# Kernel tuning notes

Hardware: AMD Instinct MI355X
Metric: run time of the kernel (lower is better)

The kernel has to match this reference:

```python
import jax, jax.numpy as jnp
import numpy as np

SEQ, B, IN, H = 512, 64, 1024, 1024


def setup_inputs() -> dict:
    key = jax.random.key(0)
    ks = jax.random.split(key, 7)
    s = 1.0 / np.sqrt(H)
    return {
        "inp": jax.random.normal(ks[0], (SEQ, B, IN), dtype=jnp.float32),
        "h0": jax.random.normal(ks[1], (1, B, H), dtype=jnp.float32),
        "c0": jax.random.normal(ks[2], (1, B, H), dtype=jnp.float32),
        "W_ih": jax.random.uniform(ks[3], (4 * H, IN), jnp.float32, -s, s),
        "W_hh": jax.random.uniform(ks[4], (4 * H, H), jnp.float32, -s, s),
        "b_ih": jax.random.uniform(ks[5], (4 * H,), jnp.float32, -s, s),
        "b_hh": jax.random.uniform(ks[6], (4 * H,), jnp.float32, -s, s),
    }


def _lstm_scan(x_bsi, h, c, W_ih, W_hh, b_ih, b_hh):
    # Precompute input projections for all timesteps in one big GEMM: (B,S,4H)
    x_proj = jnp.einsum("bsi,gi->bsg", x_bsi, W_ih) + (b_ih + b_hh)

    def step(carry, xp):
        h, c = carry  # (B,H) each; xp: (B,4H)
        gates = xp + h @ W_hh.T
        i, f, g, o = jnp.split(gates, 4, axis=-1)
        c = jax.nn.sigmoid(f) * c + jax.nn.sigmoid(i) * jnp.tanh(g)
        h = jax.nn.sigmoid(o) * jnp.tanh(c)
        return (h, c), h

    (h, c), ys = jax.lax.scan(step, (h, c), jnp.swapaxes(x_proj, 0, 1))
    return ys, h, c  # ys: (S,B,H) with ys[t] = h_t


def reference(inp, h0, c0, W_ih, W_hh, b_ih, b_hh):
    seq_len, batch, _ = inp.shape
    # Faithful to torch: .view reshapes (memory reinterpretation), NOT transpose
    x = inp.reshape(batch, seq_len, -1)          # (B,S,I)
    h = h0.reshape(batch, -1)                    # (B,H)
    c = c0.reshape(batch, -1)                    # (B,H)
    ys, h, c = _lstm_scan(x, h, c, W_ih, W_hh, b_ih, b_hh)
    # torch builds output (B,S,H) with output[:, t] = h_t, then views to (S,B,H)
    output = jnp.swapaxes(ys, 0, 1).reshape(seq_len, batch, -1)
    return output, (h.reshape(-1, batch, H), c.reshape(-1, batch, H))
```

## Files before the change

### kernel.cpp

```cpp
#include <hip/hip_runtime.h>
#include <cstdint>


typedef __bf16 bf16x8 __attribute__((ext_vector_type(8)));
typedef __bf16 bf16x4 __attribute__((ext_vector_type(4)));
typedef float  floatx4 __attribute__((ext_vector_type(4)));

#define SEQ   512
#define BATCH 64
#define HID   1024
#define GATES 4096
#define TC    128

__device__ __forceinline__ float fast_sigm(float x) {
  return 1.0f / (1.0f + __expf(-x));
}
__device__ __forceinline__ float fast_tanh(float x) {
  x = fminf(15.0f, fmaxf(-15.0f, x));
  float e = __expf(2.0f * x);
  return (e - 1.0f) / (e + 1.0f);
}

__global__ void cast_f32_to_bf16_x4(const float* __restrict__ src,
                                    __bf16* __restrict__ dst, int n4) {
  int i = blockIdx.x * blockDim.x + threadIdx.x;
  if (i < n4) {
    float4 v = reinterpret_cast<const float4*>(src)[i];
    bf16x4 o;
    o[0] = (__bf16)v.x; o[1] = (__bf16)v.y; o[2] = (__bf16)v.z; o[3] = (__bf16)v.w;
    reinterpret_cast<bf16x4*>(dst)[i] = o;
  }
}

__global__ void bias_sum(const float* __restrict__ a, const float* __restrict__ b,
                         float* __restrict__ o) {
  int i = blockIdx.x * blockDim.x + threadIdx.x;
  if (i < GATES) o[i] = a[i] + b[i];
}

__global__ __launch_bounds__(256) void gemm_xproj(
    const __bf16* __restrict__ X,
    const __bf16* __restrict__ W,
    const float*  __restrict__ bias,
    float*        __restrict__ XP,
    int t0) {
  __shared__ __bf16 As[128][40];
  __shared__ __bf16 Bs[128][40];

  const int tid  = threadIdx.x;
  const int lane = tid & 63;
  const int w    = tid >> 6;
  const int wm   = w >> 1, wn = w & 1;
  const int mt   = blockIdx.x;
  const int n0   = blockIdx.y * 128;
  const long arow0 = (long)mt * 512 + t0;

  floatx4 acc[4][4] = {};

  for (int k0 = 0; k0 < 1024; k0 += 32) {
    __syncthreads();
#pragma unroll
    for (int r = 0; r < 2; ++r) {
      int c = tid + 256 * r;
      int row = c >> 2, c8 = c & 3;
      *reinterpret_cast<uint4*>(&As[row][c8 * 8]) =
          *reinterpret_cast<const uint4*>(&X[(arow0 + row) * 1024 + k0 + c8 * 8]);
      *reinterpret_cast<uint4*>(&Bs[row][c8 * 8]) =
          *reinterpret_cast<const uint4*>(&W[(long)(n0 + row) * 1024 + k0 + c8 * 8]);
    }
    __syncthreads();

    bf16x8 a[4], b[4];
#pragma unroll
    for (int i = 0; i < 4; ++i)
      a[i] = *reinterpret_cast<const __shared__ bf16x8*>(
          &As[wm * 64 + i * 16 + (lane & 15)][(lane >> 4) * 8]);
#pragma unroll
    for (int j = 0; j < 4; ++j)
      b[j] = *reinterpret_cast<const __shared__ bf16x8*>(
          &Bs[wn * 64 + j * 16 + (lane & 15)][(lane >> 4) * 8]);
#pragma unroll
    for (int i = 0; i < 4; ++i)
#pragma unroll
      for (int j = 0; j < 4; ++j)
        acc[i][j] = __builtin_amdgcn_mfma_f32_16x16x32_bf16(a[i], b[j], acc[i][j], 0, 0, 0);
  }

#pragma unroll
  for (int i = 0; i < 4; ++i) {
    int mloc = wm * 64 + i * 16 + (lane >> 4) * 4;
#pragma unroll
    for (int j = 0; j < 4; ++j) {
      int n = n0 + wn * 64 + j * 16 + (lane & 15);
      float bn = bias[n];
#pragma unroll
      for (int r = 0; r < 4; ++r)
        XP[(long)(mt * 128 + mloc + r) * 4096 + n] = acc[i][j][r] + bn;
    }
  }
}

__global__ __launch_bounds__(256) void lstm_step(
    const __bf16* __restrict__ hin,
    __bf16*       __restrict__ hout,
    float*        __restrict__ cst,
    const __bf16* __restrict__ Whh,
    const float*  __restrict__ xp,
    float*        __restrict__ out,
    int t) {
  __shared__ __bf16 Hs[16][1032];
  __shared__ __bf16 Bs[64][264];
  __shared__ float  Gs[4][16][17];

  const int tid  = threadIdx.x;
  const int lane = tid & 63;
  const int w    = tid >> 6;
  const int j0   = blockIdx.x * 16;
  const int b0   = blockIdx.y * 16;

#pragma unroll
  for (int r = 0; r < 8; ++r) {
    int c = tid + 256 * r;
    int row = c >> 7, c8 = c & 127;
    *reinterpret_cast<uint4*>(&Hs[row][c8 * 8]) =
        *reinterpret_cast<const uint4*>(&hin[(b0 + row) * 1024 + c8 * 8]);
  }

  floatx4 acc = {};
  for (int kc = 0; kc < 4; ++kc) {
    __syncthreads();
#pragma unroll
    for (int r = 0; r < 8; ++r) {
      int c = tid + 256 * r;
      int rb = c >> 5, c8 = c & 31;
      int grow = (rb >> 4) * 1024 + j0 + (rb & 15);
      *reinterpret_cast<uint4*>(&Bs[rb][c8 * 8]) =
          *reinterpret_cast<const uint4*>(&Whh[(long)grow * 1024 + kc * 256 + c8 * 8]);
    }
    __syncthreads();
#pragma unroll
    for (int q = 0; q < 8; ++q) {
      bf16x8 a = *reinterpret_cast<const __shared__ bf16x8*>(
          &Hs[lane & 15][kc * 256 + q * 32 + (lane >> 4) * 8]);
      bf16x8 b = *reinterpret_cast<const __shared__ bf16x8*>(
          &Bs[w * 16 + (lane & 15)][q * 32 + (lane >> 4) * 8]);
      acc = __builtin_amdgcn_mfma_f32_16x16x32_bf16(a, b, acc, 0, 0, 0);
    }
  }

#pragma unroll
  for (int r = 0; r < 4; ++r)
    Gs[w][(lane >> 4) * 4 + r][lane & 15] = acc[r];
  __syncthreads();

  int bb = tid >> 4, jj = tid & 15;
  int b = b0 + bb, j = j0 + jj;
  int tt = t & (TC - 1);
  const float* xr = &xp[((long)b * TC + tt) * 4096 + j];
  float gi = Gs[0][bb][jj] + xr[0];
  float gf = Gs[1][bb][jj] + xr[1024];
  float gg = Gs[2][bb][jj] + xr[2048];
  float go = Gs[3][bb][jj] + xr[3072];
  float c_old = cst[b * 1024 + j];
  float c_new = fast_sigm(gf) * c_old + fast_sigm(gi) * fast_tanh(gg);
  float h_new = fast_sigm(go) * fast_tanh(c_new);
  cst[b * 1024 + j]  = c_new;
  hout[b * 1024 + j] = (__bf16)h_new;
  out[(long)b * (SEQ * HID) + (long)t * HID + j] = h_new;
  if (t == SEQ - 1) {
    out[(long)SEQ * BATCH * HID + b * HID + j] = h_new;
    out[(long)SEQ * BATCH * HID + BATCH * HID + b * HID + j] = c_new;
  }
}

extern "C" void kernel_launch(void* const* d_in, const int* in_sizes, int n_in,
                              void* d_out, int out_size, void* d_ws, size_t ws_size,
                              hipStream_t stream) {
  const float* inp = (const float*)d_in[0];
  const float* h0  = (const float*)d_in[1];
  const float* c0  = (const float*)d_in[2];
  const float* Wih = (const float*)d_in[3];
  const float* Whh = (const float*)d_in[4];
  const float* bih = (const float*)d_in[5];
  const float* bhh = (const float*)d_in[6];
  float* out = (float*)d_out;
  char* ws = (char*)d_ws;

  size_t off = 0;
  __bf16* Wih_b = (__bf16*)(ws + off); off += (size_t)GATES * HID * 2;
  __bf16* Whh_b = (__bf16*)(ws + off); off += (size_t)GATES * HID * 2;
  __bf16* x_b   = (__bf16*)(ws + off); off += (size_t)SEQ * BATCH * HID * 2;
  float*  xp    = (float*)(ws + off);  off += (size_t)BATCH * TC * GATES * 4;
  float*  bias  = (float*)(ws + off);  off += (size_t)GATES * 4;
  float*  cst   = (float*)(ws + off);  off += (size_t)BATCH * HID * 4;
  __bf16* hb0   = (__bf16*)(ws + off); off += (size_t)BATCH * HID * 2;
  __bf16* hb1   = (__bf16*)(ws + off); off += (size_t)BATCH * HID * 2;
  if (ws_size < off) return;

  int n4;
  n4 = GATES * HID / 4;
  cast_f32_to_bf16_x4<<<(n4 + 255) / 256, 256, 0, stream>>>(Wih, Wih_b, n4);
  cast_f32_to_bf16_x4<<<(n4 + 255) / 256, 256, 0, stream>>>(Whh, Whh_b, n4);
  n4 = SEQ * BATCH * HID / 4;
  cast_f32_to_bf16_x4<<<(n4 + 255) / 256, 256, 0, stream>>>(inp, x_b, n4);
  n4 = BATCH * HID / 4;
  cast_f32_to_bf16_x4<<<(n4 + 255) / 256, 256, 0, stream>>>(h0, hb0, n4);
  bias_sum<<<GATES / 256, 256, 0, stream>>>(bih, bhh, bias);
  hipMemcpyAsync(cst, c0, (size_t)BATCH * HID * 4, hipMemcpyDeviceToDevice, stream);

  __bf16* hbuf[2] = {hb0, hb1};
  for (int chunk = 0; chunk < SEQ / TC; ++chunk) {
    int t0 = chunk * TC;
    gemm_xproj<<<dim3(BATCH, GATES / 128), 256, 0, stream>>>(x_b, Wih_b, bias, xp, t0);
    for (int tt = 0; tt < TC; ++tt) {
      int t = t0 + tt;
      lstm_step<<<dim3(HID / 16, BATCH / 16), 256, 0, stream>>>(
          hbuf[t & 1], hbuf[(t + 1) & 1], cst, Whh_b, xp, out, t);
    }
  }
}
```

Measured before the change: 3.761 ms.

## Replace per-step LSTM launches with persistent cooperative kernel and grid barrier

```diff
diff --git a/kernel.cpp b/kernel.cpp
--- a/kernel.cpp
+++ b/kernel.cpp
@@ -11,6 +11,7 @@
 #define HID   1024
 #define GATES 4096
 #define TC    128
+#define NBLK  256
 
 __device__ __forceinline__ float fast_sigm(float x) {
   return 1.0f / (1.0f + __expf(-x));
@@ -173,6 +174,99 @@
   }
 }
 
+__global__ __launch_bounds__(256, 1) void lstm_persist(
+    const __bf16* __restrict__ Whh,
+    const float*  __restrict__ xp,
+    float*        __restrict__ cst,
+    __bf16*       __restrict__ hbuf0,
+    __bf16*       __restrict__ hbuf1,
+    float*        __restrict__ out,
+    unsigned*     __restrict__ bar,
+    int t0) {
+  __shared__ float Gp[4][4][16][17];
+
+  const int tid  = threadIdx.x;
+  const int lane = tid & 63;
+  const int w    = tid >> 6;
+  const int j0   = blockIdx.x * 16;
+  const int b0   = blockIdx.y * 16;
+
+  bf16x8 wf[32];
+  {
+    const int r = lane & 15, q = lane >> 4;
+#pragma unroll
+    for (int g = 0; g < 4; ++g)
+#pragma unroll
+      for (int k = 0; k < 8; ++k)
+        wf[g * 8 + k] = *reinterpret_cast<const bf16x8*>(
+            Whh + (size_t)(g * 1024 + j0 + r) * 1024 + (w * 8 + k) * 32 + q * 8);
+  }
+
+  const int bb = tid >> 4, jj = tid & 15;
+  const int gb = b0 + bb, gj = j0 + jj;
+  float c = cst[gb * 1024 + gj];
+
+  const int arow = (b0 + (lane & 15)) * 1024 + w * 256 + ((lane >> 4) * 8);
+  const float* xrow = xp + (size_t)gb * TC * 4096 + gj;
+  float* orow = out + (size_t)gb * (SEQ * HID) + gj;
+
+  for (int tt = 0; tt < TC; ++tt) {
+    const int t = t0 + tt;
+    const __bf16* __restrict__ hin  = (t & 1) ? hbuf1 : hbuf0;
+    __bf16*       __restrict__ hout = (t & 1) ? hbuf0 : hbuf1;
+
+    const float* xr = xrow + (size_t)tt * 4096;
+    float xi = xr[0];
+    float xf = xr[1024];
+    float xg = xr[2048];
+    float xo = xr[3072];
+
+    bf16x8 a[8];
+#pragma unroll
+    for (int k = 0; k < 8; ++k)
+      a[k] = *reinterpret_cast<const bf16x8*>(hin + arow + k * 32);
+
+    floatx4 acc[4] = {};
+#pragma unroll
+    for (int k = 0; k < 8; ++k)
+#pragma unroll
+      for (int g = 0; g < 4; ++g)
+        acc[g] = __builtin_amdgcn_mfma_f32_16x16x32_bf16(a[k], wf[g * 8 + k], acc[g], 0, 0, 0);
+
+#pragma unroll
+    for (int g = 0; g < 4; ++g)
+#pragma unroll
+      for (int r = 0; r < 4; ++r)
+        Gp[w][g][(lane >> 4) * 4 + r][lane & 15] = acc[g][r];
+    __syncthreads();
+
+    float gi = Gp[0][0][bb][jj] + Gp[1][0][bb][jj] + Gp[2][0][bb][jj] + Gp[3][0][bb][jj] + xi;
+    float gf = Gp[0][1][bb][jj] + Gp[1][1][bb][jj] + Gp[2][1][bb][jj] + Gp[3][1][bb][jj] + xf;
+    float gg = Gp[0][2][bb][jj] + Gp[1][2][bb][jj] + Gp[2][2][bb][jj] + Gp[3][2][bb][jj] + xg;
+    float go = Gp[0][3][bb][jj] + Gp[1][3][bb][jj] + Gp[2][3][bb][jj] + Gp[3][3][bb][jj] + xo;
+
+    c = fast_sigm(gf) * c + fast_sigm(gi) * fast_tanh(gg);
+    float h = fast_sigm(go) * fast_tanh(c);
+    hout[gb * 1024 + gj] = (__bf16)h;
+    orow[(size_t)t * HID] = h;
+    if (t == SEQ - 1) {
+      out[(size_t)SEQ * BATCH * HID + gb * HID + gj] = h;
+      out[(size_t)SEQ * BATCH * HID + BATCH * HID + gb * HID + gj] = c;
+    }
+
+    __syncthreads();
+    if (tid == 0) {
+      __hip_atomic_fetch_add(bar, 1u, __ATOMIC_RELEASE, __HIP_MEMORY_SCOPE_AGENT);
+      const unsigned want = (unsigned)NBLK * (unsigned)(tt + 1);
+      while (__hip_atomic_load(bar, __ATOMIC_RELAXED, __HIP_MEMORY_SCOPE_AGENT) < want) {}
+      (void)__hip_atomic_load(bar, __ATOMIC_ACQUIRE, __HIP_MEMORY_SCOPE_AGENT);
+    }
+    __syncthreads();
+  }
+
+  cst[gb * 1024 + gj] = c;
+}
+
 extern "C" void kernel_launch(void* const* d_in, const int* in_sizes, int n_in,
                               void* d_out, int out_size, void* d_ws, size_t ws_size,
                               hipStream_t stream) {
@@ -195,6 +289,7 @@
   float*  cst   = (float*)(ws + off);  off += (size_t)BATCH * HID * 4;
   __bf16* hb0   = (__bf16*)(ws + off); off += (size_t)BATCH * HID * 2;
   __bf16* hb1   = (__bf16*)(ws + off); off += (size_t)BATCH * HID * 2;
+  unsigned* bar = (unsigned*)(ws + off); off += 256;
   if (ws_size < off) return;
 
   int n4;
@@ -209,13 +304,24 @@
   hipMemcpyAsync(cst, c0, (size_t)BATCH * HID * 4, hipMemcpyDeviceToDevice, stream);
 
   __bf16* hbuf[2] = {hb0, hb1};
+  bool coop_ok = true;
   for (int chunk = 0; chunk < SEQ / TC; ++chunk) {
     int t0 = chunk * TC;
     gemm_xproj<<<dim3(BATCH, GATES / 128), 256, 0, stream>>>(x_b, Wih_b, bias, xp, t0);
-    for (int tt = 0; tt < TC; ++tt) {
-      int t = t0 + tt;
-      lstm_step<<<dim3(HID / 16, BATCH / 16), 256, 0, stream>>>(
-          hbuf[t & 1], hbuf[(t + 1) & 1], cst, Whh_b, xp, out, t);
-    }
-  }
-}
+    if (coop_ok) {
+      hipMemsetAsync(bar, 0, sizeof(unsigned), stream);
+      void* args[] = {(void*)&Whh_b, (void*)&xp, (void*)&cst, (void*)&hb0,
+                      (void*)&hb1, (void*)&out, (void*)&bar, (void*)&t0};
+      if (hipLaunchCooperativeKernel((const void*)lstm_persist, dim3(64, 4),
+                                     dim3(256, 1, 1), args, 0, stream) != hipSuccess)
+        coop_ok = false;
+    }
+    if (!coop_ok) {
+      for (int tt = 0; tt < TC; ++tt) {
+        int t = t0 + tt;
+        lstm_step<<<dim3(HID / 16, BATCH / 16), 256, 0, stream>>>(
+            hbuf[t & 1], hbuf[(t + 1) & 1], cst, Whh_b, xp, out, t);
+      }
+    }
+  }
+}
```

New measurement: 8.246 ms. +119.3%, slower.
